# Kernel optimization log

Measured on AMD Instinct MI355X. Metric: run time of the kernel, lower is better.

The kernel has to match this reference:

```python
import jax, jax.numpy as jnp
import numpy as np

N_S = 50000
N_T = 50000
N = N_S + N_T
D = 128
NEG_SLOPE = 0.2


def gat_conv(x, src, dst, W, a_src, a_dst, n_nodes):
    """PyG GATConv, heads=1, bias=False, add_self_loops=True (loops already appended by caller? no: here)."""
    h = x @ W.T                                   # [N, out]
    loops = jnp.arange(n_nodes, dtype=src.dtype)
    src = jnp.concatenate([src, loops])
    dst = jnp.concatenate([dst, loops])
    a_s = h @ a_src                               # [N]
    a_d = h @ a_dst                               # [N]
    e = jax.nn.leaky_relu(a_s[src] + a_d[dst], NEG_SLOPE)   # [E]
    e_max = jax.ops.segment_max(e, dst, num_segments=n_nodes)
    e = jnp.exp(e - e_max[dst])
    denom = jax.ops.segment_sum(e, dst, num_segments=n_nodes)
    alpha = e / (denom[dst] + 1e-16)
    out = jax.ops.segment_sum(h[src] * alpha[:, None], dst, num_segments=n_nodes)
    return out


def setup_inputs() -> dict:
    key = jax.random.key(0)
    ks = jax.random.split(key, 16)
    E = 500000
    edge_index = jax.random.randint(ks[0], (2, E), 0, N_S, dtype=jnp.int64)
    paper_edge_index = jax.random.randint(ks[1], (2, E), 0, N, dtype=jnp.int64)
    author_edge_index = jax.random.randint(ks[2], (2, E), 0, N, dtype=jnp.int64)
    x_s = jax.random.normal(ks[3], (N_S, D), dtype=jnp.float32)
    x_t = jax.random.normal(ks[4], (N_T, D), dtype=jnp.float32)
    s = 1.0 / np.sqrt(D)
    return {
        "edge_index": edge_index,
        "paper_edge_index": paper_edge_index,
        "author_edge_index": author_edge_index,
        "x_s": x_s,
        "x_t": x_t,
        "Ws": jax.random.normal(ks[5], (D, D), dtype=jnp.float32) * s,
        "bs": jax.random.normal(ks[6], (D,), dtype=jnp.float32) * s,
        "Wt": jax.random.normal(ks[7], (D, D), dtype=jnp.float32) * s,
        "bt": jax.random.normal(ks[8], (D,), dtype=jnp.float32) * s,
        "W1": jax.random.normal(ks[9], (D, D), dtype=jnp.float32) * s,
        "a1s": jax.random.normal(ks[10], (D,), dtype=jnp.float32) * s,
        "a1d": jax.random.normal(ks[11], (D,), dtype=jnp.float32) * s,
        "W2": jax.random.normal(ks[12], (D, D), dtype=jnp.float32) * s,
        "a2s": jax.random.normal(ks[13], (D,), dtype=jnp.float32) * s,
        "a2d": jax.random.normal(ks[14], (D,), dtype=jnp.float32) * s,
    }


def reference(edge_index, paper_edge_index, author_edge_index, x_s, x_t,
              Ws, bs, Wt, bt, W1, a1s, a1d, W2, a2s, a2d):
    # training=None -> no dropout
    x_s = x_s @ Ws.T + bs
    x_t = x_t @ Wt.T + bt
    src = edge_index[0]
    dst = edge_index[1] + N_S  # reindex target nodes into concatenated space
    x = jnp.concatenate([x_s, x_t], axis=0)  # [N, D]

    # conv_1: bipartite edges s->t plus author-author edges
    src1 = jnp.concatenate([src, author_edge_index[0]])
    dst1 = jnp.concatenate([dst, author_edge_index[1]])
    new_x_t = jax.nn.relu(gat_conv(x, src1, dst1, W1, a1s, a1d, N))

    # conv_2: transposed bipartite edges t->s plus paper-paper edges
    src2 = jnp.concatenate([dst, paper_edge_index[0]])
    dst2 = jnp.concatenate([src, paper_edge_index[1]])
    new_x_s = jax.nn.relu(gat_conv(x, src2, dst2, W2, a2s, a2d, N))

    return (new_x_s[:N_S], new_x_t[N_S:])
```

## Files before the change

kernel.cpp:

```cpp
#include <hip/hip_runtime.h>
#include <hip/hip_bf16.h>

#define E0   500000
#define NS   50000
#define DD   128
#define ETOT (2*E0 + NS)

#define GEMM_BLOCKS 1564
#define EDGE_BLOCKS 4102

#define OFF_H1    0UL
#define OFF_H2    6400000UL
#define OFF_AS1   12800000UL
#define OFF_AD1   12900000UL
#define OFF_AS2   13000000UL
#define OFF_AD2   13100000UL
#define OFF_DEG1  13200000UL
#define OFF_DEG2  13250000UL
#define OFF_RP1   13300000UL
#define OFF_RP2   13351000UL
#define OFF_PS    13402000UL
#define OFF_PREF  13402128UL
#define OFF_SLOT1 13402256UL
#define OFF_SLOT2 14452256UL
#define OFF_REC1  15502256UL
#define OFF_REC2  16552256UL

typedef __bf16 bf16x8 __attribute__((ext_vector_type(8)));
typedef float f32x4 __attribute__((ext_vector_type(4)));

__device__ __forceinline__ ushort f2bf(float f) {
    uint b = __float_as_uint(f);
    return (ushort)((b + 0x7FFFu + ((b >> 16) & 1u)) >> 16);
}
__device__ __forceinline__ uint pk2(float a, float b) {
    return (uint)f2bf(a) | ((uint)f2bf(b) << 16);
}

__device__ __forceinline__ void stage_w_bf16(ushort* Wl, const float* __restrict__ W, int tid) {
#pragma unroll
    for (int i = 0; i < 8; i++) {
        const int idx = i * 256 + tid;
        const int row = idx >> 4, ch = idx & 15;
        const float4 f0 = *(const float4*)(W + row * DD + ch * 8);
        const float4 f1 = *(const float4*)(W + row * DD + ch * 8 + 4);
        uint4 v = make_uint4(pk2(f0.x, f0.y), pk2(f0.z, f0.w), pk2(f1.x, f1.y), pk2(f1.z, f1.w));
        *(uint4*)((char*)Wl + ((row * 256 + ch * 16) ^ ((row & 7) << 4))) = v;
    }
}

__device__ __forceinline__ void stage_x(ushort* Xl, const float* __restrict__ xin,
                                        int row0, int tid) {
#pragma unroll
    for (int i = 0; i < 4; i++) {
        const int idx = i * 256 + tid;
        const int r = idx >> 4, ch = idx & 15;
        const int gr = row0 + r;
        float4 f0 = make_float4(0.f, 0.f, 0.f, 0.f), f1 = f0;
        if (gr < NS) {
            f0 = *(const float4*)(xin + (size_t)gr * DD + ch * 8);
            f1 = *(const float4*)(xin + (size_t)gr * DD + ch * 8 + 4);
        }
        uint4 v = make_uint4(pk2(f0.x, f0.y), pk2(f0.z, f0.w), pk2(f1.x, f1.y), pk2(f1.z, f1.w));
        *(uint4*)((char*)Xl + ((r * 256 + ch * 16) ^ ((r & 7) << 4))) = v;
    }
}

__device__ __forceinline__ void mfma_phase(const ushort* Wl, const ushort* Xl,
                                           int wrow, int lane, f32x4 acc[8]) {
    const int l15 = lane & 15, q = lane >> 4;
    bf16x8 a[4];
#pragma unroll
    for (int ks = 0; ks < 4; ks++) {
        const int row = wrow + l15;
        const int byte = (row * 256 + (ks * 32 + q * 8) * 2) ^ ((row & 7) << 4);
        a[ks] = *(const bf16x8*)((const char*)Xl + byte);
    }
#pragma unroll
    for (int nt = 0; nt < 8; nt++) {
        const int n = nt * 16 + l15;
#pragma unroll
        for (int ks = 0; ks < 4; ks++) {
            const int byte = (n * 256 + (ks * 32 + q * 8) * 2) ^ ((n & 7) << 4);
            bf16x8 b = *(const bf16x8*)((const char*)Wl + byte);
            acc[nt] = __builtin_amdgcn_mfma_f32_16x16x32_bf16(a[ks], b, acc[nt], 0, 0, 0);
        }
    }
}

__device__ __forceinline__ void epi23(const f32x4 acc[8], int half, int row0, int wrow,
                                      int lane, const float* __restrict__ avs,
                                      const float* __restrict__ avd,
                                      ushort* __restrict__ h,
                                      float* __restrict__ as_, float* __restrict__ ad_) {
    const int l15 = lane & 15, q = lane >> 4;
    float vs[8], vd[8];
#pragma unroll
    for (int nt = 0; nt < 8; nt++) { vs[nt] = avs[nt * 16 + l15]; vd[nt] = avd[nt * 16 + l15]; }
#pragma unroll
    for (int r = 0; r < 4; r++) {
        const int gr = row0 + wrow + q * 4 + r;
        const bool ok = gr < NS;
        const size_t node = (size_t)(half * NS + gr);
        float ps = 0.f, pd = 0.f;
#pragma unroll
        for (int nt = 0; nt < 8; nt++) {
            const float v = acc[nt][r];
            ps += v * vs[nt];
            pd += v * vd[nt];
            if (ok) h[node * DD + nt * 16 + l15] = f2bf(v);
        }
#pragma unroll
        for (int m = 8; m; m >>= 1) { ps += __shfl_xor(ps, m); pd += __shfl_xor(pd, m); }
        if (ok && l15 == 0) { as_[node] = ps; ad_[node] = pd; }
    }
}

__global__ __launch_bounds__(256) void k_fat(
    const float* __restrict__ xs, const float* __restrict__ xt,
    const float* __restrict__ Ws, const float* __restrict__ bs,
    const float* __restrict__ Wt, const float* __restrict__ bt,
    const float* __restrict__ W1, const float* __restrict__ a1s, const float* __restrict__ a1d,
    const float* __restrict__ W2, const float* __restrict__ a2s, const float* __restrict__ a2d,
    ushort* __restrict__ h1, ushort* __restrict__ h2,
    float* __restrict__ as1, float* __restrict__ ad1,
    float* __restrict__ as2, float* __restrict__ ad2,
    const int* __restrict__ ei, const int* __restrict__ pei, const int* __restrict__ aei,
    int* __restrict__ deg1, int* __restrict__ deg2,
    int* __restrict__ slot1, int* __restrict__ slot2) {
    __shared__ __align__(16) ushort Wl[128 * 128];
    __shared__ __align__(16) ushort Xl[64 * 128];
    const int bid = blockIdx.x;
    const int tid = threadIdx.x;

    if (bid >= GEMM_BLOCKS) {
        const int e = (bid - GEMM_BLOCKS) * 256 + tid;
        if (e >= ETOT) return;
        if (e < E0) {
            const int a = ei[e], b = ei[E0 + e];
            slot1[e] = atomicAdd(&deg1[b], 1);
            slot2[e] = atomicAdd(&deg2[a], 1);
        } else if (e < 2 * E0) {
            const int k = e - E0;
            const int d1 = aei[E0 + k];
            if (d1 >= NS) slot1[e] = atomicAdd(&deg1[d1 - NS], 1);
            const int d2 = pei[E0 + k];
            if (d2 < NS) slot2[e] = atomicAdd(&deg2[d2], 1);
        } else {
            const int k = e - 2 * E0;
            slot1[e] = atomicAdd(&deg1[k], 1);
            slot2[e] = atomicAdd(&deg2[k], 1);
        }
        return;
    }

    const int lane = tid & 63, wv = tid >> 6, wrow = wv * 16;
    const int l15 = lane & 15, q = lane >> 4;
    const int half = (bid >= 782) ? 1 : 0;
    const int row0 = (bid - half * 782) * 64;
    const float* xin = half ? xt : xs;
    const float* W0  = half ? Wt : Ws;
    const float* b0  = half ? bt : bs;

    stage_w_bf16(Wl, W0, tid);
    stage_x(Xl, xin, row0, tid);
    __syncthreads();

    f32x4 acc[8];
#pragma unroll
    for (int nt = 0; nt < 8; nt++) acc[nt] = 0.f;
    mfma_phase(Wl, Xl, wrow, lane, acc);

#pragma unroll
    for (int nt = 0; nt < 8; nt++) {
        const float bvv = b0[nt * 16 + l15];
#pragma unroll
        for (int r = 0; r < 4; r++) {
            const int row = wrow + q * 4 + r;
            const int byte = (row * 256 + (nt * 16 + l15) * 2) ^ ((row & 7) << 4);
            *(ushort*)((char*)Xl + byte) = f2bf(acc[nt][r] + bvv);
        }
    }
    __syncthreads();
    stage_w_bf16(Wl, W1, tid);
    __syncthreads();

#pragma unroll
    for (int nt = 0; nt < 8; nt++) acc[nt] = 0.f;
    mfma_phase(Wl, Xl, wrow, lane, acc);
    epi23(acc, half, row0, wrow, lane, a1s, a1d, h1, as1, ad1);

    __syncthreads();
    stage_w_bf16(Wl, W2, tid);
    __syncthreads();

#pragma unroll
    for (int nt = 0; nt < 8; nt++) acc[nt] = 0.f;
    mfma_phase(Wl, Xl, wrow, lane, acc);
    epi23(acc, half, row0, wrow, lane, a2s, a2d, h2, as2, ad2);
}

__device__ __forceinline__ int wave_incl_scan(int x, int lane) {
#pragma unroll
    for (int off = 1; off < 64; off <<= 1) {
        const int v = __shfl_up(x, off);
        if (lane >= off) x += v;
    }
    return x;
}

__device__ __forceinline__ int4 load_deg4(const int* __restrict__ d, int idx) {
    if (idx + 3 < NS) return *(const int4*)(d + idx);
    int4 v = make_int4(0, 0, 0, 0);
    if (idx + 0 < NS) v.x = d[idx + 0];
    if (idx + 1 < NS) v.y = d[idx + 1];
    if (idx + 2 < NS) v.z = d[idx + 2];
    if (idx + 3 < NS) v.w = d[idx + 3];
    return v;
}

__global__ __launch_bounds__(256) void k_scan1(const int* __restrict__ deg,
                                               int* __restrict__ psum) {
    const int conv = blockIdx.y, blk = blockIdx.x, t = threadIdx.x;
    const int* d = deg + conv * NS;
    const int4 v = load_deg4(d, blk * 1024 + t * 4);
    int s = v.x + v.y + v.z + v.w;
#pragma unroll
    for (int m = 32; m; m >>= 1) s += __shfl_xor(s, m);
    __shared__ int wsum[4];
    const int lane = t & 63, wv = t >> 6;
    if (lane == 0) wsum[wv] = s;
    __syncthreads();
    if (t == 0) psum[conv * 64 + blk] = wsum[0] + wsum[1] + wsum[2] + wsum[3];
}

__global__ __launch_bounds__(128) void k_scan2(const int* __restrict__ psum,
                                               int* __restrict__ pref) {
    const int t = threadIdx.x;
    const int w = t >> 6, lane = t & 63;
    const int x = (lane < 49) ? psum[w * 64 + lane] : 0;
    const int incl = wave_incl_scan(x, lane);
    if (lane < 49) pref[w * 64 + lane] = incl - x;
}

__global__ __launch_bounds__(256) void k_scan3(const int* __restrict__ deg,
                                               const int* __restrict__ pref,
                                               int* __restrict__ rp1, int* __restrict__ rp2) {
    const int conv = blockIdx.y, blk = blockIdx.x, t = threadIdx.x;
    const int* d = deg + conv * NS;
    int* rp = conv ? rp2 : rp1;
    const int idx = blk * 1024 + t * 4;
    const int4 v = load_deg4(d, idx);
    const int tsum = v.x + v.y + v.z + v.w;
    const int lane = t & 63, wv = t >> 6;
    const int incl = wave_incl_scan(tsum, lane);
    __shared__ int wsum[4];
    if (lane == 63) wsum[wv] = incl;
    __syncthreads();
    int woff = 0;
#pragma unroll
    for (int i = 0; i < 4; i++) woff += (i < wv) ? wsum[i] : 0;
    int ex = pref[conv * 64 + blk] + woff + (incl - tsum);
    if (idx + 0 < NS) rp[idx + 0] = ex; ex += v.x;
    if (idx + 1 < NS) rp[idx + 1] = ex; ex += v.y;
    if (idx + 2 < NS) rp[idx + 2] = ex; ex += v.z;
    if (idx + 3 < NS) rp[idx + 3] = ex; ex += v.w;
    if (blk == 48 && t == 0)
        rp[NS] = pref[conv * 64 + 48] + wsum[0] + wsum[1] + wsum[2] + wsum[3];
}

__global__ __launch_bounds__(256) void k_fill(
    const int* __restrict__ ei, const int* __restrict__ pei, const int* __restrict__ aei,
    const int* __restrict__ rp1, const int* __restrict__ rp2,
    const int* __restrict__ slot1, const int* __restrict__ slot2,
    int* __restrict__ rec1, int* __restrict__ rec2) {
    const int e = blockIdx.x * 256 + threadIdx.x;
    if (e >= ETOT) return;
    if (e < E0) {
        const int a = ei[e], b = ei[E0 + e];
        rec1[rp1[b] + slot1[e]] = a;
        rec2[rp2[a] + slot2[e]] = b + NS;
    } else if (e < 2 * E0) {
        const int k = e - E0;
        const int s1 = aei[k], d1 = aei[E0 + k];
        if (d1 >= NS) rec1[rp1[d1 - NS] + slot1[e]] = s1;
        const int s2 = pei[k], d2 = pei[E0 + k];
        if (d2 < NS) rec2[rp2[d2] + slot2[e]] = s2;
    } else {
        const int k = e - 2 * E0;
        rec1[rp1[k] + slot1[e]] = NS + k;
        rec2[rp2[k] + slot2[e]] = k;
    }
}

__device__ __forceinline__ void fma8(float acc[8], float e, const uint4 q) {
    acc[0] += e * __uint_as_float(q.x << 16);
    acc[1] += e * __uint_as_float(q.x & 0xFFFF0000u);
    acc[2] += e * __uint_as_float(q.y << 16);
    acc[3] += e * __uint_as_float(q.y & 0xFFFF0000u);
    acc[4] += e * __uint_as_float(q.z << 16);
    acc[5] += e * __uint_as_float(q.z & 0xFFFF0000u);
    acc[6] += e * __uint_as_float(q.w << 16);
    acc[7] += e * __uint_as_float(q.w & 0xFFFF0000u);
}

__global__ __launch_bounds__(256) void k_gather(
    const int* __restrict__ rp1, const int* __restrict__ rec1, const ushort* __restrict__ h1,
    const float* __restrict__ as1, const float* __restrict__ ad1,
    const int* __restrict__ rp2, const int* __restrict__ rec2, const ushort* __restrict__ h2,
    const float* __restrict__ as2, const float* __restrict__ ad2,
    float* __restrict__ out) {
    const int conv = blockIdx.y;
    const int* rp = conv ? rp2 : rp1;
    const int* rec = conv ? rec2 : rec1;
    const ushort* h = conv ? h2 : h1;
    const float* as_ = conv ? as2 : as1;
    const float* ad_ = conv ? ad2 : ad1;
    float* outb = conv ? out : out + (size_t)NS * DD;
    const int node = blockIdx.x * 4 + (threadIdx.x >> 6);
    const int gd = conv ? node : node + NS;
    const int lane = threadIdx.x & 63;
    const int g = lane >> 4, l16 = lane & 15;
    const int beg = rp[node], end = rp[node + 1];
    const float adv = ad_[gd];
    float acc[8];
#pragma unroll
    for (int i = 0; i < 8; i++) acc[i] = 0.f;
    float es = 0.f;

    for (int e0 = beg + g * 4; e0 < end; e0 += 16) {
        int s[4];
#pragma unroll
        for (int u = 0; u < 4; u++)
            s[u] = (e0 + u < end) ? rec[e0 + u] : 0;
        uint4 q[4];
#pragma unroll
        for (int u = 0; u < 4; u++)
            q[u] = *(const uint4*)(h + (size_t)s[u] * DD + l16 * 8);
        float w[4];
#pragma unroll
        for (int u = 0; u < 4; u++) {
            float ev = as_[s[u]] + adv;
            ev = ev > 0.f ? ev : 0.2f * ev;
            w[u] = (e0 + u < end) ? __expf(ev) : 0.f;
        }
#pragma unroll
        for (int u = 0; u < 4; u++) {
            es += w[u];
            fma8(acc, w[u], q[u]);
        }
    }

#pragma unroll
    for (int i = 0; i < 8; i++) {
        acc[i] += __shfl_xor(acc[i], 16);
        acc[i] += __shfl_xor(acc[i], 32);
    }
    es += __shfl_xor(es, 16);
    es += __shfl_xor(es, 32);

    if (g == 0) {
        const float inv = 1.f / (es + 1e-16f);
        float4 o0, o1;
        o0.x = fmaxf(acc[0] * inv, 0.f);
        o0.y = fmaxf(acc[1] * inv, 0.f);
        o0.z = fmaxf(acc[2] * inv, 0.f);
        o0.w = fmaxf(acc[3] * inv, 0.f);
        o1.x = fmaxf(acc[4] * inv, 0.f);
        o1.y = fmaxf(acc[5] * inv, 0.f);
        o1.z = fmaxf(acc[6] * inv, 0.f);
        o1.w = fmaxf(acc[7] * inv, 0.f);
        *(float4*)(outb + (size_t)node * DD + l16 * 8) = o0;
        *(float4*)(outb + (size_t)node * DD + l16 * 8 + 4) = o1;
    }
}

extern "C" void kernel_launch(void* const* d_in, const int* in_sizes, int n_in,
                              void* d_out, int out_size, void* d_ws, size_t ws_size,
                              hipStream_t stream) {
    const int* ei  = (const int*)d_in[0];
    const int* pei = (const int*)d_in[1];
    const int* aei = (const int*)d_in[2];
    const float* xs  = (const float*)d_in[3];
    const float* xt  = (const float*)d_in[4];
    const float* Ws  = (const float*)d_in[5];
    const float* bs  = (const float*)d_in[6];
    const float* Wt  = (const float*)d_in[7];
    const float* bt  = (const float*)d_in[8];
    const float* W1  = (const float*)d_in[9];
    const float* a1s = (const float*)d_in[10];
    const float* a1d = (const float*)d_in[11];
    const float* W2  = (const float*)d_in[12];
    const float* a2s = (const float*)d_in[13];
    const float* a2d = (const float*)d_in[14];
    float* ws  = (float*)d_ws;
    float* out = (float*)d_out;

    ushort* h1 = (ushort*)(ws + OFF_H1);
    ushort* h2 = (ushort*)(ws + OFF_H2);
    float* as1 = ws + OFF_AS1;
    float* ad1 = ws + OFF_AD1;
    float* as2 = ws + OFF_AS2;
    float* ad2 = ws + OFF_AD2;
    int* deg1  = (int*)(ws + OFF_DEG1);
    int* rp1   = (int*)(ws + OFF_RP1);
    int* rp2   = (int*)(ws + OFF_RP2);
    int* psum  = (int*)(ws + OFF_PS);
    int* pref  = (int*)(ws + OFF_PREF);
    int* slot1 = (int*)(ws + OFF_SLOT1);
    int* slot2 = (int*)(ws + OFF_SLOT2);
    int* rec1  = (int*)(ws + OFF_REC1);
    int* rec2  = (int*)(ws + OFF_REC2);

    hipMemsetAsync(deg1, 0, 2 * NS * sizeof(int), stream);

    k_fat<<<GEMM_BLOCKS + EDGE_BLOCKS, 256, 0, stream>>>(
        xs, xt, Ws, bs, Wt, bt, W1, a1s, a1d, W2, a2s, a2d,
        h1, h2, as1, ad1, as2, ad2,
        ei, pei, aei, deg1, deg1 + NS, slot1, slot2);

    k_scan1<<<dim3(49, 2), 256, 0, stream>>>(deg1, psum);
    k_scan2<<<1, 128, 0, stream>>>(psum, pref);
    k_scan3<<<dim3(49, 2), 256, 0, stream>>>(deg1, pref, rp1, rp2);

    k_fill<<<EDGE_BLOCKS, 256, 0, stream>>>(ei, pei, aei, rp1, rp2, slot1, slot2, rec1, rec2);

    k_gather<<<dim3(NS / 4, 2), 256, 0, stream>>>(
        rp1, rec1, h1, as1, ad1, rp2, rec2, h2, as2, ad2, out);
}
```

Before: 318.0 us.

## Fuse scan, fill and gather into one cooperative kernel; interleave GEMM and edge blocks

Replaces the five launches after the fused GEMM/degree kernel (three scan passes, CSR fill, gather) with a single cooperative persistent kernel. Inside it, grid-wide syncs separate the phases, which removes the per-launch overhead and tail gaps between them. The first kernel's block mapping is also changed to interleave 3 GEMM tiles with 8 edge-counting blocks per group, so atomics overlap with MFMA work across the GPU. The risks are the cost of grid.sync and lower occupancy for the gather phase with a fixed 1792-block grid. If the cooperative launch fails, it falls back to the separate kernels.

Measured after the change: 1.123 ms. +253.2%, slower.

```diff
diff --git a/kernel.cpp b/kernel.cpp
--- a/kernel.cpp
+++ b/kernel.cpp
@@ -1,13 +1,19 @@
 #include <hip/hip_runtime.h>
 #include <hip/hip_bf16.h>
+#include <hip/hip_cooperative_groups.h>
+
+namespace cg = cooperative_groups;
 
 #define E0   500000
 #define NS   50000
 #define DD   128
 #define ETOT (2*E0 + NS)
 
-#define GEMM_BLOCKS 1564
+#define GEMM_TILES  1564
 #define EDGE_BLOCKS 4102
+#define FAT_GROUPS  522
+#define FAT_BLOCKS  (FAT_GROUPS * 11)
+#define MEGA_BLOCKS 1792
 
 #define OFF_H1    0UL
 #define OFF_H2    6400000UL
@@ -132,9 +138,12 @@
     __shared__ __align__(16) ushort Xl[64 * 128];
     const int bid = blockIdx.x;
     const int tid = threadIdx.x;
-
-    if (bid >= GEMM_BLOCKS) {
-        const int e = (bid - GEMM_BLOCKS) * 256 + tid;
+    const int g = bid / 11, r = bid % 11;
+
+    if (r >= 3) {
+        const int eb = g * 8 + (r - 3);
+        if (eb >= EDGE_BLOCKS) return;
+        const int e = eb * 256 + tid;
         if (e >= ETOT) return;
         if (e < E0) {
             const int a = ei[e], b = ei[E0 + e];
@@ -154,10 +163,12 @@
         return;
     }
 
+    const int tile = g * 3 + r;
+    if (tile >= GEMM_TILES) return;
     const int lane = tid & 63, wv = tid >> 6, wrow = wv * 16;
     const int l15 = lane & 15, q = lane >> 4;
-    const int half = (bid >= 782) ? 1 : 0;
-    const int row0 = (bid - half * 782) * 64;
+    const int half = (tile >= 782) ? 1 : 0;
+    const int row0 = (tile - half * 782) * 64;
     const float* xin = half ? xt : xs;
     const float* W0  = half ? Wt : Ws;
     const float* b0  = half ? bt : bs;
@@ -175,10 +186,10 @@
     for (int nt = 0; nt < 8; nt++) {
         const float bvv = b0[nt * 16 + l15];
 #pragma unroll
-        for (int r = 0; r < 4; r++) {
-            const int row = wrow + q * 4 + r;
+        for (int rr = 0; rr < 4; rr++) {
+            const int row = wrow + q * 4 + rr;
             const int byte = (row * 256 + (nt * 16 + l15) * 2) ^ ((row & 7) << 4);
-            *(ushort*)((char*)Xl + byte) = f2bf(acc[nt][r] + bvv);
+            *(ushort*)((char*)Xl + byte) = f2bf(acc[nt][rr] + bvv);
         }
     }
     __syncthreads();
@@ -219,63 +230,11 @@
     return v;
 }
 
-__global__ __launch_bounds__(256) void k_scan1(const int* __restrict__ deg,
-                                               int* __restrict__ psum) {
-    const int conv = blockIdx.y, blk = blockIdx.x, t = threadIdx.x;
-    const int* d = deg + conv * NS;
-    const int4 v = load_deg4(d, blk * 1024 + t * 4);
-    int s = v.x + v.y + v.z + v.w;
-#pragma unroll
-    for (int m = 32; m; m >>= 1) s += __shfl_xor(s, m);
-    __shared__ int wsum[4];
-    const int lane = t & 63, wv = t >> 6;
-    if (lane == 0) wsum[wv] = s;
-    __syncthreads();
-    if (t == 0) psum[conv * 64 + blk] = wsum[0] + wsum[1] + wsum[2] + wsum[3];
-}
-
-__global__ __launch_bounds__(128) void k_scan2(const int* __restrict__ psum,
-                                               int* __restrict__ pref) {
-    const int t = threadIdx.x;
-    const int w = t >> 6, lane = t & 63;
-    const int x = (lane < 49) ? psum[w * 64 + lane] : 0;
-    const int incl = wave_incl_scan(x, lane);
-    if (lane < 49) pref[w * 64 + lane] = incl - x;
-}
-
-__global__ __launch_bounds__(256) void k_scan3(const int* __restrict__ deg,
-                                               const int* __restrict__ pref,
-                                               int* __restrict__ rp1, int* __restrict__ rp2) {
-    const int conv = blockIdx.y, blk = blockIdx.x, t = threadIdx.x;
-    const int* d = deg + conv * NS;
-    int* rp = conv ? rp2 : rp1;
-    const int idx = blk * 1024 + t * 4;
-    const int4 v = load_deg4(d, idx);
-    const int tsum = v.x + v.y + v.z + v.w;
-    const int lane = t & 63, wv = t >> 6;
-    const int incl = wave_incl_scan(tsum, lane);
-    __shared__ int wsum[4];
-    if (lane == 63) wsum[wv] = incl;
-    __syncthreads();
-    int woff = 0;
-#pragma unroll
-    for (int i = 0; i < 4; i++) woff += (i < wv) ? wsum[i] : 0;
-    int ex = pref[conv * 64 + blk] + woff + (incl - tsum);
-    if (idx + 0 < NS) rp[idx + 0] = ex; ex += v.x;
-    if (idx + 1 < NS) rp[idx + 1] = ex; ex += v.y;
-    if (idx + 2 < NS) rp[idx + 2] = ex; ex += v.z;
-    if (idx + 3 < NS) rp[idx + 3] = ex; ex += v.w;
-    if (blk == 48 && t == 0)
-        rp[NS] = pref[conv * 64 + 48] + wsum[0] + wsum[1] + wsum[2] + wsum[3];
-}
-
-__global__ __launch_bounds__(256) void k_fill(
-    const int* __restrict__ ei, const int* __restrict__ pei, const int* __restrict__ aei,
+__device__ __forceinline__ void fill_edge(
+    int e, const int* __restrict__ ei, const int* __restrict__ pei, const int* __restrict__ aei,
     const int* __restrict__ rp1, const int* __restrict__ rp2,
     const int* __restrict__ slot1, const int* __restrict__ slot2,
     int* __restrict__ rec1, int* __restrict__ rec2) {
-    const int e = blockIdx.x * 256 + threadIdx.x;
-    if (e >= ETOT) return;
     if (e < E0) {
         const int a = ei[e], b = ei[E0 + e];
         rec1[rp1[b] + slot1[e]] = a;
@@ -304,22 +263,20 @@
     acc[7] += e * __uint_as_float(q.w & 0xFFFF0000u);
 }
 
-__global__ __launch_bounds__(256) void k_gather(
+__device__ __forceinline__ void gather_node(
+    int conv, int node, int lane,
     const int* __restrict__ rp1, const int* __restrict__ rec1, const ushort* __restrict__ h1,
     const float* __restrict__ as1, const float* __restrict__ ad1,
     const int* __restrict__ rp2, const int* __restrict__ rec2, const ushort* __restrict__ h2,
     const float* __restrict__ as2, const float* __restrict__ ad2,
     float* __restrict__ out) {
-    const int conv = blockIdx.y;
     const int* rp = conv ? rp2 : rp1;
     const int* rec = conv ? rec2 : rec1;
     const ushort* h = conv ? h2 : h1;
     const float* as_ = conv ? as2 : as1;
     const float* ad_ = conv ? ad2 : ad1;
     float* outb = conv ? out : out + (size_t)NS * DD;
-    const int node = blockIdx.x * 4 + (threadIdx.x >> 6);
     const int gd = conv ? node : node + NS;
-    const int lane = threadIdx.x & 63;
     const int g = lane >> 4, l16 = lane & 15;
     const int beg = rp[node], end = rp[node + 1];
     const float adv = ad_[gd];
@@ -373,6 +330,150 @@
         *(float4*)(outb + (size_t)node * DD + l16 * 8) = o0;
         *(float4*)(outb + (size_t)node * DD + l16 * 8 + 4) = o1;
     }
+}
+
+__global__ __launch_bounds__(256, 8) void k_mega(
+    const int* __restrict__ ei, const int* __restrict__ pei, const int* __restrict__ aei,
+    int* __restrict__ deg1,
+    int* __restrict__ psum, int* __restrict__ pref,
+    int* __restrict__ rp1, int* __restrict__ rp2,
+    const int* __restrict__ slot1, const int* __restrict__ slot2,
+    int* __restrict__ rec1, int* __restrict__ rec2,
+    const ushort* __restrict__ h1, const ushort* __restrict__ h2,
+    const float* __restrict__ as1, const float* __restrict__ ad1,
+    const float* __restrict__ as2, const float* __restrict__ ad2,
+    float* __restrict__ out) {
+    cg::grid_group grid = cg::this_grid();
+    __shared__ int wsum[4];
+    const int bid = blockIdx.x, t = threadIdx.x;
+    const int lane = t & 63, wv = t >> 6;
+
+    if (bid < 98) {
+        const int conv = bid / 49, blk = bid % 49;
+        const int* d = deg1 + conv * NS;
+        const int4 v = load_deg4(d, blk * 1024 + t * 4);
+        int s = v.x + v.y + v.z + v.w;
+#pragma unroll
+        for (int m = 32; m; m >>= 1) s += __shfl_xor(s, m);
+        if (lane == 0) wsum[wv] = s;
+        __syncthreads();
+        if (t == 0) psum[conv * 64 + blk] = wsum[0] + wsum[1] + wsum[2] + wsum[3];
+    }
+    grid.sync();
+
+    if (bid == 0 && t < 128) {
+        const int w = t >> 6, l = t & 63;
+        const int x = (l < 49) ? psum[w * 64 + l] : 0;
+        const int incl = wave_incl_scan(x, l);
+        if (l < 49) pref[w * 64 + l] = incl - x;
+    }
+    grid.sync();
+
+    if (bid < 98) {
+        const int conv = bid / 49, blk = bid % 49;
+        const int* d = deg1 + conv * NS;
+        int* rp = conv ? rp2 : rp1;
+        const int idx = blk * 1024 + t * 4;
+        const int4 v = load_deg4(d, idx);
+        const int tsum = v.x + v.y + v.z + v.w;
+        const int incl = wave_incl_scan(tsum, lane);
+        if (lane == 63) wsum[wv] = incl;
+        __syncthreads();
+        int woff = 0;
+#pragma unroll
+        for (int i = 0; i < 4; i++) woff += (i < wv) ? wsum[i] : 0;
+        int ex = pref[conv * 64 + blk] + woff + (incl - tsum);
+        if (idx + 0 < NS) rp[idx + 0] = ex; ex += v.x;
+        if (idx + 1 < NS) rp[idx + 1] = ex; ex += v.y;
+        if (idx + 2 < NS) rp[idx + 2] = ex; ex += v.z;
+        if (idx + 3 < NS) rp[idx + 3] = ex; ex += v.w;
+        if (blk == 48 && t == 0)
+            rp[NS] = pref[conv * 64 + 48] + wsum[0] + wsum[1] + wsum[2] + wsum[3];
+    }
+    grid.sync();
+
+    for (int e = bid * 256 + t; e < ETOT; e += gridDim.x * 256)
+        fill_edge(e, ei, pei, aei, rp1, rp2, slot1, slot2, rec1, rec2);
+    grid.sync();
+
+    for (int grp = bid; grp < 25000; grp += gridDim.x) {
+        const int conv = grp / 12500;
+        const int node = (grp - conv * 12500) * 4 + wv;
+        gather_node(conv, node, lane, rp1, rec1, h1, as1, ad1,
+                    rp2, rec2, h2, as2, ad2, out);
+    }
+}
+
+__global__ __launch_bounds__(256) void k_scan1(const int* __restrict__ deg,
+                                               int* __restrict__ psum) {
+    const int conv = blockIdx.y, blk = blockIdx.x, t = threadIdx.x;
+    const int* d = deg + conv * NS;
+    const int4 v = load_deg4(d, blk * 1024 + t * 4);
+    int s = v.x + v.y + v.z + v.w;
+#pragma unroll
+    for (int m = 32; m; m >>= 1) s += __shfl_xor(s, m);
+    __shared__ int wsum[4];
+    const int lane = t & 63, wv = t >> 6;
+    if (lane == 0) wsum[wv] = s;
+    __syncthreads();
+    if (t == 0) psum[conv * 64 + blk] = wsum[0] + wsum[1] + wsum[2] + wsum[3];
+}
+
+__global__ __launch_bounds__(128) void k_scan2(const int* __restrict__ psum,
+                                               int* __restrict__ pref) {
+    const int t = threadIdx.x;
+    const int w = t >> 6, lane = t & 63;
+    const int x = (lane < 49) ? psum[w * 64 + lane] : 0;
+    const int incl = wave_incl_scan(x, lane);
+    if (lane < 49) pref[w * 64 + lane] = incl - x;
+}
+
+__global__ __launch_bounds__(256) void k_scan3(const int* __restrict__ deg,
+                                               const int* __restrict__ pref,
+                                               int* __restrict__ rp1, int* __restrict__ rp2) {
+    const int conv = blockIdx.y, blk = blockIdx.x, t = threadIdx.x;
+    const int* d = deg + conv * NS;
+    int* rp = conv ? rp2 : rp1;
+    const int idx = blk * 1024 + t * 4;
+    const int4 v = load_deg4(d, idx);
+    const int tsum = v.x + v.y + v.z + v.w;
+    const int lane = t & 63, wv = t >> 6;
+    const int incl = wave_incl_scan(tsum, lane);
+    __shared__ int wsum[4];
+    if (lane == 63) wsum[wv] = incl;
+    __syncthreads();
+    int woff = 0;
+#pragma unroll
+    for (int i = 0; i < 4; i++) woff += (i < wv) ? wsum[i] : 0;
+    int ex = pref[conv * 64 + blk] + woff + (incl - tsum);
+    if (idx + 0 < NS) rp[idx + 0] = ex; ex += v.x;
+    if (idx + 1 < NS) rp[idx + 1] = ex; ex += v.y;
+    if (idx + 2 < NS) rp[idx + 2] = ex; ex += v.z;
+    if (idx + 3 < NS) rp[idx + 3] = ex; ex += v.w;
+    if (blk == 48 && t == 0)
+        rp[NS] = pref[conv * 64 + 48] + wsum[0] + wsum[1] + wsum[2] + wsum[3];
+}
+
+__global__ __launch_bounds__(256) void k_fill(
+    const int* __restrict__ ei, const int* __restrict__ pei, const int* __restrict__ aei,
+    const int* __restrict__ rp1, const int* __restrict__ rp2,
+    const int* __restrict__ slot1, const int* __restrict__ slot2,
+    int* __restrict__ rec1, int* __restrict__ rec2) {
+    const int e = blockIdx.x * 256 + threadIdx.x;
+    if (e >= ETOT) return;
+    fill_edge(e, ei, pei, aei, rp1, rp2, slot1, slot2, rec1, rec2);
+}
+
+__global__ __launch_bounds__(256) void k_gather(
+    const int* __restrict__ rp1, const int* __restrict__ rec1, const ushort* __restrict__ h1,
+    const float* __restrict__ as1, const float* __restrict__ ad1,
+    const int* __restrict__ rp2, const int* __restrict__ rec2, const ushort* __restrict__ h2,
+    const float* __restrict__ as2, const float* __restrict__ ad2,
+    float* __restrict__ out) {
+    const int conv = blockIdx.y;
+    const int node = blockIdx.x * 4 + (threadIdx.x >> 6);
+    gather_node(conv, node, threadIdx.x & 63, rp1, rec1, h1, as1, ad1,
+                rp2, rec2, h2, as2, ad2, out);
 }
 
 extern "C" void kernel_launch(void* const* d_in, const int* in_sizes, int n_in,
@@ -414,17 +515,28 @@
 
     hipMemsetAsync(deg1, 0, 2 * NS * sizeof(int), stream);
 
-    k_fat<<<GEMM_BLOCKS + EDGE_BLOCKS, 256, 0, stream>>>(
+    k_fat<<<FAT_BLOCKS, 256, 0, stream>>>(
         xs, xt, Ws, bs, Wt, bt, W1, a1s, a1d, W2, a2s, a2d,
         h1, h2, as1, ad1, as2, ad2,
         ei, pei, aei, deg1, deg1 + NS, slot1, slot2);
 
-    k_scan1<<<dim3(49, 2), 256, 0, stream>>>(deg1, psum);
-    k_scan2<<<1, 128, 0, stream>>>(psum, pref);
-    k_scan3<<<dim3(49, 2), 256, 0, stream>>>(deg1, pref, rp1, rp2);
-
-    k_fill<<<EDGE_BLOCKS, 256, 0, stream>>>(ei, pei, aei, rp1, rp2, slot1, slot2, rec1, rec2);
-
-    k_gather<<<dim3(NS / 4, 2), 256, 0, stream>>>(
-        rp1, rec1, h1, as1, ad1, rp2, rec2, h2, as2, ad2, out);
-}
+    void* margs[] = {
+        (void*)&ei, (void*)&pei, (void*)&aei,
+        (void*)&deg1, (void*)&psum, (void*)&pref,
+        (void*)&rp1, (void*)&rp2, (void*)&slot1, (void*)&slot2,
+        (void*)&rec1, (void*)&rec2,
+        (void*)&h1, (void*)&h2,
+        (void*)&as1, (void*)&ad1, (void*)&as2, (void*)&ad2,
+        (void*)&out
+    };
+    hipError_t merr = hipLaunchCooperativeKernel((const void*)k_mega, dim3(MEGA_BLOCKS),
+                                                 dim3(256), margs, 0, stream);
+    if (merr != hipSuccess) {
+        k_scan1<<<dim3(49, 2), 256, 0, stream>>>(deg1, psum);
+        k_scan2<<<1, 128, 0, stream>>>(psum, pref);
+        k_scan3<<<dim3(49, 2), 256, 0, stream>>>(deg1, pref, rp1, rp2);
+        k_fill<<<EDGE_BLOCKS, 256, 0, stream>>>(ei, pei, aei, rp1, rp2, slot1, slot2, rec1, rec2);
+        k_gather<<<dim3(NS / 4, 2), 256, 0, stream>>>(
+            rp1, rec1, h1, as1, ad1, rp2, rec2, h2, as2, ad2, out);
+    }
+}
```
